# Kernel optimization log

Hardware: AMD Instinct MI355X
Metric: run time of the kernel (lower is better)

Reference implementation:

```python
import jax, jax.numpy as jnp
import numpy as np

N_NODES = 50000
N_EDGES = 800000
HID = 128
N_PROC = 3  # num_layers - 1 processor iterations (shared weights)


def _mlp(x, w1, b1, w2, b2, w3, b3):
    h = jax.nn.relu(x @ w1 + b1)
    h = jax.nn.relu(h @ w2 + b2)
    return h @ w3 + b3


def setup_inputs() -> dict:
    key = jax.random.key(0)
    ks = jax.random.split(key, 32)

    def p(k, shape):
        fan_in = shape[0]
        return (jax.random.normal(k, shape, dtype=jnp.float32) / np.float32(np.sqrt(fan_in)))

    inp = {
        "X_curr": jax.random.normal(ks[0], (N_NODES, 6), dtype=jnp.float32),
        "y_prev": jax.random.normal(ks[1], (N_NODES,), dtype=jnp.float32),
        "edge": jax.random.randint(ks[2], (2, N_EDGES), 0, N_NODES, dtype=jnp.int32),
        "mode": 0,
        # EdgeModel net: Linear(9,H) ReLU Linear(H,H) ReLU Linear(H,3)
        "ew1": p(ks[3], (9, HID)), "eb1": jnp.zeros((HID,), jnp.float32),
        "ew2": p(ks[4], (HID, HID)), "eb2": jnp.zeros((HID,), jnp.float32),
        "ew3": p(ks[5], (HID, 3)), "eb3": jnp.zeros((3,), jnp.float32),
        # NodeModel net: Linear(5,H) ReLU Linear(H,H) ReLU Linear(H,1)
        "nw1": p(ks[6], (5, HID)), "nb1": jnp.zeros((HID,), jnp.float32),
        "nw2": p(ks[7], (HID, HID)), "nb2": jnp.zeros((HID,), jnp.float32),
        "nw3": p(ks[8], (HID, 1)), "nb3": jnp.zeros((1,), jnp.float32),
        # decoder: Linear(5,H) ReLU Linear(H,H) ReLU Linear(H,H) ReLU Linear(H,1)
        "dw1": p(ks[9], (5, HID)), "db1": jnp.zeros((HID,), jnp.float32),
        "dw2": p(ks[10], (HID, HID)), "db2": jnp.zeros((HID,), jnp.float32),
        "dw3": p(ks[11], (HID, HID)), "db3": jnp.zeros((HID,), jnp.float32),
        "dw4": p(ks[12], (HID, 1)), "db4": jnp.zeros((1,), jnp.float32),
    }
    return inp


def reference(X_curr, y_prev,
              ew1, eb1, ew2, eb2, ew3, eb3,
              nw1, nb1, nw2, nb2, nw3, nb3,
              dw1, db1, dw2, db2, dw3, db3, dw4, db4,
              edge, mode):
    n = X_curr.shape[0]
    src_idx, dst_idx = edge[0], edge[1]
    # x_in = cat(X_curr[:, [0,1,2,4]], y_prev)  -> [N, 5]
    x = jnp.concatenate([X_curr[:, jnp.array([0, 1, 2, 4])], y_prev[:, None]], axis=-1)

    # _compute_edge_attr: grad_r = (f_dest - f_src) * disp_r
    xs, xd = x[src_idx], x[dst_idx]
    disp = xd[:, :3] - xs[:, :3]
    edge_attr = (xd[:, 4] - xs[:, 4])[:, None] * disp  # [E, 3]

    # degree for scatter-mean (nodes with no incoming edges aggregate to 0)
    deg = jax.ops.segment_sum(jnp.ones((edge.shape[1],), x.dtype), dst_idx, num_segments=n)
    inv_deg = jnp.where(deg > 0, 1.0 / jnp.maximum(deg, 1.0), 0.0)

    for _ in range(N_PROC):
        # EdgeModel
        xs, xd = x[src_idx], x[dst_idx]
        disp = xd[:, :3] - xs[:, :3]
        norm_r = jnp.linalg.norm(disp, axis=-1, keepdims=True)
        net_in = jnp.concatenate([disp, norm_r, edge_attr, xs[:, 4:5], xd[:, 4:5]], axis=-1)  # [E, 9]
        edge_attr = edge_attr + _mlp(net_in, ew1, eb1, ew2, eb2, ew3, eb3)
        # NodeModel: message = edge_attr, aggr='mean' at target (edge[1])
        aggr = jax.ops.segment_sum(edge_attr, dst_idx, num_segments=n) * inv_deg[:, None]  # [N, 3]
        node_in = jnp.concatenate([x[:, 3:5], aggr], axis=-1)  # [N, 5]
        delta = _mlp(node_in, nw1, nb1, nw2, nb2, nw3, nb3)[:, 0]
        x = x.at[:, 4].add(delta)

    # decoder
    h = jax.nn.relu(x @ dw1 + db1)
    h = jax.nn.relu(h @ dw2 + db2)
    h = jax.nn.relu(h @ dw3 + db3)
    x_out = h @ dw4 + db4  # [N, 1]
    return y_prev + x_out[:, 0]
```

## Files before the change

kernel.cpp:

```cpp
#include <hip/hip_runtime.h>

typedef float f32x4 __attribute__((ext_vector_type(4)));
typedef __bf16 bf16x8 __attribute__((ext_vector_type(8)));
typedef __bf16 bf16x4 __attribute__((ext_vector_type(4)));

#define WB_W1E 0
#define WB_W2E 4096
#define WB_W3E 20480
#define WB_W1N 22528
#define WB_W2N 26624
#define WB_W3N 43008
#define WB_W1D 45056
#define WB_W2D 49152
#define WB_W3D 65536
#define WB_W4D 81920
#define WB_TOTAL 83968

#define BKT_SHIFT 6
#define BKT_SZ 64

__global__ void k_prep(const float* __restrict__ ew1, const float* __restrict__ eb1,
                       const float* __restrict__ ew2, const float* __restrict__ ew3,
                       const float* __restrict__ nw1, const float* __restrict__ nb1,
                       const float* __restrict__ nw2, const float* __restrict__ nw3,
                       const float* __restrict__ dw1, const float* __restrict__ db1,
                       const float* __restrict__ dw2, const float* __restrict__ dw3,
                       const float* __restrict__ dw4, __bf16* __restrict__ wb) {
  int gid = blockIdx.x * 256 + threadIdx.x;
  if (gid >= WB_TOTAL) return;
  const float* srcs[10] = {ew1, ew2, ew3, nw1, nw2, nw3, dw1, dw2, dw3, dw4};
  const float* brow[10] = {eb1, 0, 0, nb1, 0, 0, db1, 0, 0, 0};
  const int Ks[10] = {9, 128, 128, 5, 128, 128, 5, 128, 128, 128};
  const int Ns[10] = {128, 128, 3, 128, 128, 1, 128, 128, 128, 1};
  const int CTs[10] = {8, 8, 1, 8, 8, 1, 8, 8, 8, 1};
  const int cum[11] = {0, 4096, 20480, 22528, 26624, 43008, 45056, 49152, 65536, 81920, 83968};
  int seg = 0;
  while (gid >= cum[seg + 1]) seg++;
  int li = gid - cum[seg];
  int j = li & 7;
  int lane = (li >> 3) & 63;
  int fi = li >> 9;
  int CT = CTs[seg];
  int ct = fi % CT;
  int kt = fi / CT;
  int k = kt * 32 + ((lane >> 4) << 3) + j;
  int n = ct * 16 + (lane & 15);
  int kl;
  if (seg == 0) {
    if (k < 4) kl = k;
    else if (k >= 8 && k < 13) kl = k - 4;
    else kl = (k == 13) ? -2 : -1;
  } else if (seg == 3 || seg == 6) {
    if (k < 5) kl = k;
    else kl = (k == 5) ? -2 : -1;
  } else {
    kl = (k < Ks[seg]) ? k : -1;
  }
  float v = 0.f;
  if (n < Ns[seg]) {
    if (kl >= 0) v = srcs[seg][kl * Ns[seg] + n];
    else if (kl == -2 && brow[seg]) v = brow[seg][n];
  }
  wb[gid] = (__bf16)v;
}

__global__ void k_zero(const float* __restrict__ y_prev, float* __restrict__ x4,
                       int* __restrict__ bcnt, int n, int nbkt) {
  int i = blockIdx.x * 256 + threadIdx.x;
  if (i < n) x4[i] = y_prev[i];
  if (i <= nbkt) bcnt[i] = 0;
}

__global__ __launch_bounds__(256) void k_cntb(const int* __restrict__ dstp,
                                              int* __restrict__ bcnt, int nbkt, int E) {
  __shared__ int hist[1024];
  int tid = threadIdx.x;
  for (int t = tid; t < nbkt; t += 256) hist[t] = 0;
  __syncthreads();
  int e0 = blockIdx.x * 8192;
#pragma unroll
  for (int j = 0; j < 32; j++) {
    int e = e0 + j * 256 + tid;
    if (e < E) atomicAdd(&hist[dstp[e] >> BKT_SHIFT], 1);
  }
  __syncthreads();
  for (int t = tid; t < nbkt; t += 256) {
    int c = hist[t];
    if (c) atomicAdd(&bcnt[t], c);
  }
}

__global__ void k_scanb(const int* __restrict__ bcnt, int* __restrict__ bstart,
                        int* __restrict__ cur, int* __restrict__ rp, int nbkt, int n, int E) {
  __shared__ int sd[1024];
  int t = threadIdx.x;
  int c = (t < nbkt) ? bcnt[t] : 0;
  sd[t] = c;
  __syncthreads();
#pragma unroll
  for (int off = 1; off < 1024; off <<= 1) {
    int v = sd[t];
    int u = (t >= off) ? sd[t - off] : 0;
    __syncthreads();
    sd[t] = v + u;
    __syncthreads();
  }
  if (t < nbkt) {
    int ex = sd[t] - c;
    bstart[t] = ex;
    cur[t] = ex;
  }
  if (t == 0) {
    bstart[nbkt] = E;
    rp[n] = E;
  }
}

__global__ __launch_bounds__(256) void k_bin(const int* __restrict__ dstp, int* __restrict__ cur,
                                             int* __restrict__ eix, int nbkt, int E) {
  __shared__ int hist[1024];
  __shared__ int base[1024];
  int tid = threadIdx.x;
  for (int t = tid; t < nbkt; t += 256) hist[t] = 0;
  __syncthreads();
  int e0 = blockIdx.x * 8192;
  int b[32], lr[32];
#pragma unroll
  for (int j = 0; j < 32; j++) {
    int e = e0 + j * 256 + tid;
    if (e < E) {
      b[j] = dstp[e] >> BKT_SHIFT;
      lr[j] = atomicAdd(&hist[b[j]], 1);
    } else {
      b[j] = -1;
      lr[j] = 0;
    }
  }
  __syncthreads();
  for (int t = tid; t < nbkt; t += 256) {
    int c = hist[t];
    base[t] = c ? atomicAdd(&cur[t], c) : 0;
  }
  __syncthreads();
#pragma unroll
  for (int j = 0; j < 32; j++)
    if (b[j] >= 0) eix[base[b[j]] + lr[j]] = e0 + j * 256 + tid;
}

__global__ __launch_bounds__(256) void k_build(const int* __restrict__ srcO,
                                               const int* __restrict__ dstO,
                                               const float* __restrict__ Xc,
                                               const float* __restrict__ yp,
                                               const int* __restrict__ bstart, const int* eix,
                                               int* __restrict__ srcS, int* dstS,
                                               float* __restrict__ peS, float* __restrict__ eaS,
                                               int* __restrict__ rp, float* __restrict__ invdeg,
                                               int n) {
  __shared__ int cnt[BKT_SZ];
  __shared__ int starts[BKT_SZ];
  int tid = threadIdx.x;
  int d0 = blockIdx.x << BKT_SHIFT;
  if (tid < BKT_SZ) cnt[tid] = 0;
  int gstart = bstart[blockIdx.x], gend = bstart[blockIdx.x + 1];
  __syncthreads();
  int ei[16], dd[16], rr[16];
#pragma unroll
  for (int k = 0; k < 16; k++) {
    int p = gstart + k * 256 + tid;
    ei[k] = (p < gend) ? eix[p] : -1;
  }
#pragma unroll
  for (int k = 0; k < 16; k++) {
    if (ei[k] >= 0) {
      dd[k] = dstO[ei[k]];
      rr[k] = atomicAdd(&cnt[dd[k] - d0], 1);
    }
  }
  __syncthreads();
  if (tid < 64) {
    int c = cnt[tid];
    int s = c;
#pragma unroll
    for (int off = 1; off < 64; off <<= 1) {
      int u = __shfl_up(s, off);
      if (tid >= off) s += u;
    }
    int ex = s - c;
    starts[tid] = ex;
    int d = d0 + tid;
    if (d < n) {
      rp[d] = gstart + ex;
      invdeg[d] = c > 0 ? 1.0f / (float)c : 0.f;
    }
  }
  __syncthreads();
#pragma unroll
  for (int k = 0; k < 16; k++) {
    int e = ei[k];
    if (e < 0) continue;
    int s = srcO[e], d = dd[k];
    float dx = Xc[d * 6 + 0] - Xc[s * 6 + 0];
    float dy = Xc[d * 6 + 1] - Xc[s * 6 + 1];
    float dz = Xc[d * 6 + 2] - Xc[s * 6 + 2];
    float nr = sqrtf(dx * dx + dy * dy + dz * dz);
    float w = yp[d] - yp[s];
    int q = gstart + starts[d - d0] + rr[k];
    srcS[q] = s;
    dstS[q] = d;
    f32x4 pv = {dx, dy, dz, nr};
    *(f32x4*)(peS + 4 * q) = pv;
    f32x4 av = {w * dx, w * dy, w * dz, 0.f};
    *(f32x4*)(eaS + 4 * q) = av;
  }
}

__device__ __forceinline__ int aoff(int row, int b) { return (row * 256 + b) ^ ((row & 15) << 4); }

__device__ __forceinline__ void wg_sync() {
  asm volatile("s_waitcnt lgkmcnt(0)" ::: "memory");
  __builtin_amdgcn_s_barrier();
}

__device__ __forceinline__ bf16x4 relu_pack(f32x4 a) {
  bf16x4 p;
#pragma unroll
  for (int r = 0; r < 4; r++) {
    float v = a[r];
    p[r] = (__bf16)(v > 0.f ? v : 0.f);
  }
  return p;
}

__global__ __attribute__((amdgpu_flat_work_group_size(256, 256), amdgpu_waves_per_eu(3, 4))) void
k_edge(const float* __restrict__ x4, const float* __restrict__ pe, float* __restrict__ ea,
       const int* __restrict__ src, const int* __restrict__ dstp,
       const __bf16* __restrict__ W1f, const __bf16* __restrict__ W2f,
       const __bf16* __restrict__ W3f, const float* __restrict__ b2,
       const float* __restrict__ b3, int ntiles, int E) {
  __shared__ char Ab[16384];
  __shared__ char Bb[16384];
  const int tid = threadIdx.x;
  const int l = tid & 63, w = tid >> 6;
  const int col = l & 15, krow = l >> 4;
  const int rl = w * 16 + (l >> 2), chunk = l & 3;

  bf16x8 w1r[2], w2r[4][2], w3r[4];
#pragma unroll
  for (int t = 0; t < 2; t++) w1r[t] = *(const bf16x8*)(W1f + ((2 * w + t) << 9) + l * 8);
#pragma unroll
  for (int kt = 0; kt < 4; kt++)
#pragma unroll
    for (int t = 0; t < 2; t++)
      w2r[kt][t] = *(const bf16x8*)(W2f + ((kt * 8 + 2 * w + t) << 9) + l * 8);
#pragma unroll
  for (int kt = 0; kt < 4; kt++) w3r[kt] = *(const bf16x8*)(W3f + (kt << 9) + l * 8);
  f32x4 b2c[2];
#pragma unroll
  for (int t = 0; t < 2; t++) b2c[t] = *(const f32x4*)(b2 + (2 * w + t) * 16 + krow * 4);
  f32x4 b3i = {0.f, 0.f, 0.f, 0.f};
  if (krow == 0) {
    b3i[0] = b3[0];
    b3i[1] = b3[1];
    b3i[2] = b3[2];
  }

  int tile = blockIdx.x;
  if (tile >= ntiles) return;

  int e0 = tile * 64 + rl;
  int ec = e0 < E ? e0 : E - 1;
  int cs = src[ec], cd = dstp[ec];
  f32x4 cld = {0.f, 0.f, 0.f, 0.f};
  if (chunk < 2) cld = *(const f32x4*)(((chunk == 1) ? ea : pe) + 4 * ec);
  float cxs = 0.f, cxd = 0.f;
  if (chunk == 1) {
    cxs = x4[cs];
    cxd = x4[cd];
  }

  for (;;) {
    bf16x8 v;
#pragma unroll
    for (int q = 0; q < 8; q++) v[q] = (__bf16)0.f;
    if (chunk == 0) {
      v[0] = (__bf16)cld[0];
      v[1] = (__bf16)cld[1];
      v[2] = (__bf16)cld[2];
      v[3] = (__bf16)cld[3];
    } else if (chunk == 1) {
      v[0] = (__bf16)cld[0];
      v[1] = (__bf16)cld[1];
      v[2] = (__bf16)cld[2];
      v[3] = (__bf16)cxs;
      v[4] = (__bf16)cxd;
      v[5] = (__bf16)1.0f;
    }
    *(bf16x8*)(Ab + aoff(rl, chunk * 16)) = v;

    int nt = tile + (int)gridDim.x;
    bool hn = nt < ntiles;
    int tc = hn ? nt : tile;
    int en = tc * 64 + rl;
    if (en >= E) en = E - 1;
    int ns = src[en], nd = dstp[en];

    wg_sync();

    f32x4 h[4][2];
#pragma unroll
    for (int c = 0; c < 4; c++)
#pragma unroll
      for (int t = 0; t < 2; t++) {
        f32x4 z = {0.f, 0.f, 0.f, 0.f};
        h[c][t] = z;
      }
    bf16x8 bb[4];
#pragma unroll
    for (int c = 0; c < 4; c++) bb[c] = *(const bf16x8*)(Ab + aoff(c * 16 + col, krow * 16));
#pragma unroll
    for (int c = 0; c < 4; c++)
#pragma unroll
      for (int t = 0; t < 2; t++)
        h[c][t] = __builtin_amdgcn_mfma_f32_16x16x32_bf16(w1r[t], bb[c], h[c][t], 0, 0, 0);
#pragma unroll
    for (int c = 0; c < 4; c++)
#pragma unroll
      for (int t = 0; t < 2; t++)
        *(bf16x4*)(Bb + aoff(c * 16 + col, (2 * w + t) * 32 + krow * 8)) = relu_pack(h[c][t]);

    wg_sync();

    f32x4 nld = {0.f, 0.f, 0.f, 0.f};
    if (chunk < 2) nld = *(const f32x4*)(((chunk == 1) ? ea : pe) + 4 * en);
    float nxs = 0.f, nxd = 0.f;
    if (chunk == 1) {
      nxs = x4[ns];
      nxd = x4[nd];
    }

#pragma unroll
    for (int c = 0; c < 4; c++)
#pragma unroll
      for (int t = 0; t < 2; t++) h[c][t] = b2c[t];
#pragma unroll
    for (int kt = 0; kt < 4; kt++) {
#pragma unroll
      for (int c = 0; c < 4; c++)
        bb[c] = *(const bf16x8*)(Bb + aoff(c * 16 + col, kt * 64 + krow * 16));
#pragma unroll
      for (int c = 0; c < 4; c++)
#pragma unroll
        for (int t = 0; t < 2; t++)
          h[c][t] = __builtin_amdgcn_mfma_f32_16x16x32_bf16(w2r[kt][t], bb[c], h[c][t], 0, 0, 0);
    }
#pragma unroll
    for (int c = 0; c < 4; c++)
#pragma unroll
      for (int t = 0; t < 2; t++)
        *(bf16x4*)(Ab + aoff(c * 16 + col, (2 * w + t) * 32 + krow * 8)) = relu_pack(h[c][t]);

    wg_sync();

    f32x4 o = b3i;
#pragma unroll
    for (int kt = 0; kt < 4; kt++) {
      bf16x8 bq = *(const bf16x8*)(Ab + aoff(w * 16 + col, kt * 64 + krow * 16));
      o = __builtin_amdgcn_mfma_f32_16x16x32_bf16(w3r[kt], bq, o, 0, 0, 0);
    }

    if (krow == 0) {
      int e3 = tile * 64 + w * 16 + col;
      if (e3 < E) {
        f32x4 oe = *(const f32x4*)(ea + 4 * e3);
        f32x4 nv;
        nv[0] = oe[0] + o[0];
        nv[1] = oe[1] + o[1];
        nv[2] = oe[2] + o[2];
        nv[3] = 0.f;
        *(f32x4*)(ea + 4 * e3) = nv;
      }
    }

    if (!hn) break;
    tile = nt;
    cld = nld;
    cxs = nxs;
    cxd = nxd;
  }
}

__global__ __attribute__((amdgpu_flat_work_group_size(256, 256), amdgpu_waves_per_eu(3, 4))) void
k_node(float* __restrict__ x4, const float* __restrict__ Xc, const float* __restrict__ eaS,
       const int* __restrict__ rp, const float* __restrict__ invdeg,
       const __bf16* __restrict__ W1f, const __bf16* __restrict__ W2f,
       const __bf16* __restrict__ W3f, const float* __restrict__ b2,
       const float* __restrict__ b3, int n) {
  __shared__ char Ab[16384];
  __shared__ char Bb[16384];
  const int tid = threadIdx.x;
  const int l = tid & 63, w = tid >> 6;
  const int col = l & 15, krow = l >> 4;
  const int rl = w * 16 + (l >> 2), chunk = l & 3;

  bf16x8 w1r[2], w2r[4][2], w3r[4];
#pragma unroll
  for (int t = 0; t < 2; t++) w1r[t] = *(const bf16x8*)(W1f + ((2 * w + t) << 9) + l * 8);
#pragma unroll
  for (int kt = 0; kt < 4; kt++)
#pragma unroll
    for (int t = 0; t < 2; t++)
      w2r[kt][t] = *(const bf16x8*)(W2f + ((kt * 8 + 2 * w + t) << 9) + l * 8);
#pragma unroll
  for (int kt = 0; kt < 4; kt++) w3r[kt] = *(const bf16x8*)(W3f + (kt << 9) + l * 8);
  f32x4 b2c[2];
#pragma unroll
  for (int t = 0; t < 2; t++) b2c[t] = *(const f32x4*)(b2 + (2 * w + t) * 16 + krow * 4);
  float b3s = b3[0];

  int tile = blockIdx.x;
  int i0 = tile * 64 + rl;
  bool vi = i0 < n;
  int i = vi ? i0 : (n - 1);

  int ss = rp[i], se = rp[i + 1];
  float a0 = 0.f, a1 = 0.f, a2 = 0.f;
  for (int p = ss + chunk; p < se; p += 4) {
    f32x4 ev = *(const f32x4*)(eaS + 4 * p);
    a0 += ev[0];
    a1 += ev[1];
    a2 += ev[2];
  }
  a0 += __shfl_xor(a0, 1);
  a1 += __shfl_xor(a1, 1);
  a2 += __shfl_xor(a2, 1);
  a0 += __shfl_xor(a0, 2);
  a1 += __shfl_xor(a1, 2);
  a2 += __shfl_xor(a2, 2);

  bf16x8 v;
#pragma unroll
  for (int q = 0; q < 8; q++) v[q] = (__bf16)0.f;
  if (chunk == 0) {
    float x3 = Xc[i * 6 + 4];
    float xv = x4[i];
    float iv = invdeg[i];
    v[0] = (__bf16)x3;
    v[1] = (__bf16)xv;
    v[2] = (__bf16)(a0 * iv);
    v[3] = (__bf16)(a1 * iv);
    v[4] = (__bf16)(a2 * iv);
    v[5] = (__bf16)1.0f;
  }
  *(bf16x8*)(Ab + aoff(rl, chunk * 16)) = v;

  wg_sync();

  f32x4 h[4][2];
#pragma unroll
  for (int c = 0; c < 4; c++)
#pragma unroll
    for (int t = 0; t < 2; t++) {
      f32x4 z = {0.f, 0.f, 0.f, 0.f};
      h[c][t] = z;
    }
  bf16x8 bb[4];
#pragma unroll
  for (int c = 0; c < 4; c++) bb[c] = *(const bf16x8*)(Ab + aoff(c * 16 + col, krow * 16));
#pragma unroll
  for (int c = 0; c < 4; c++)
#pragma unroll
    for (int t = 0; t < 2; t++)
      h[c][t] = __builtin_amdgcn_mfma_f32_16x16x32_bf16(w1r[t], bb[c], h[c][t], 0, 0, 0);
#pragma unroll
  for (int c = 0; c < 4; c++)
#pragma unroll
    for (int t = 0; t < 2; t++)
      *(bf16x4*)(Bb + aoff(c * 16 + col, (2 * w + t) * 32 + krow * 8)) = relu_pack(h[c][t]);

  wg_sync();

#pragma unroll
  for (int c = 0; c < 4; c++)
#pragma unroll
    for (int t = 0; t < 2; t++) h[c][t] = b2c[t];
#pragma unroll
  for (int kt = 0; kt < 4; kt++) {
#pragma unroll
    for (int c = 0; c < 4; c++)
      bb[c] = *(const bf16x8*)(Bb + aoff(c * 16 + col, kt * 64 + krow * 16));
#pragma unroll
    for (int c = 0; c < 4; c++)
#pragma unroll
      for (int t = 0; t < 2; t++)
        h[c][t] = __builtin_amdgcn_mfma_f32_16x16x32_bf16(w2r[kt][t], bb[c], h[c][t], 0, 0, 0);
  }
#pragma unroll
  for (int c = 0; c < 4; c++)
#pragma unroll
    for (int t = 0; t < 2; t++)
      *(bf16x4*)(Ab + aoff(c * 16 + col, (2 * w + t) * 32 + krow * 8)) = relu_pack(h[c][t]);

  wg_sync();

  f32x4 o = {0.f, 0.f, 0.f, 0.f};
  if (krow == 0) o[0] = b3s;
#pragma unroll
  for (int kt = 0; kt < 4; kt++) {
    bf16x8 bq = *(const bf16x8*)(Ab + aoff(w * 16 + col, kt * 64 + krow * 16));
    o = __builtin_amdgcn_mfma_f32_16x16x32_bf16(w3r[kt], bq, o, 0, 0, 0);
  }

  if (krow == 0) {
    int i3 = tile * 64 + w * 16 + col;
    if (i3 < n) x4[i3] = x4[i3] + o[0];
  }
}

__global__ __attribute__((amdgpu_flat_work_group_size(256, 256), amdgpu_waves_per_eu(2, 4))) void
k_dec(const float* __restrict__ x4, const float* __restrict__ Xc, const float* __restrict__ y_prev,
      const __bf16* __restrict__ W1f, const __bf16* __restrict__ W2f,
      const __bf16* __restrict__ W3f, const __bf16* __restrict__ W4f,
      const float* __restrict__ b2, const float* __restrict__ b3, const float* __restrict__ b4,
      float* __restrict__ out, int n) {
  __shared__ char Ab[16384];
  __shared__ char Bb[16384];
  const int tid = threadIdx.x;
  const int l = tid & 63, w = tid >> 6;
  const int col = l & 15, krow = l >> 4;
  const int rl = w * 16 + (l >> 2), chunk = l & 3;

  bf16x8 w1r[2], w2r[4][2], w3r[4][2], w4r[4];
#pragma unroll
  for (int t = 0; t < 2; t++) w1r[t] = *(const bf16x8*)(W1f + ((2 * w + t) << 9) + l * 8);
#pragma unroll
  for (int kt = 0; kt < 4; kt++)
#pragma unroll
    for (int t = 0; t < 2; t++) {
      w2r[kt][t] = *(const bf16x8*)(W2f + ((kt * 8 + 2 * w + t) << 9) + l * 8);
      w3r[kt][t] = *(const bf16x8*)(W3f + ((kt * 8 + 2 * w + t) << 9) + l * 8);
    }
#pragma unroll
  for (int kt = 0; kt < 4; kt++) w4r[kt] = *(const bf16x8*)(W4f + (kt << 9) + l * 8);
  f32x4 b2c[2], b3c[2];
#pragma unroll
  for (int t = 0; t < 2; t++) {
    b2c[t] = *(const f32x4*)(b2 + (2 * w + t) * 16 + krow * 4);
    b3c[t] = *(const f32x4*)(b3 + (2 * w + t) * 16 + krow * 4);
  }
  float b4s = b4[0];

  int tile = blockIdx.x;
  int i0 = tile * 64 + rl;
  bool vi = i0 < n;
  int i = vi ? i0 : (n - 1);

  bf16x8 v;
#pragma unroll
  for (int q = 0; q < 8; q++) v[q] = (__bf16)0.f;
  if (chunk == 0) {
    v[0] = (__bf16)Xc[i * 6 + 0];
    v[1] = (__bf16)Xc[i * 6 + 1];
    v[2] = (__bf16)Xc[i * 6 + 2];
    v[3] = (__bf16)Xc[i * 6 + 4];
    v[4] = (__bf16)x4[i];
    v[5] = (__bf16)1.0f;
  }
  *(bf16x8*)(Ab + aoff(rl, chunk * 16)) = v;

  wg_sync();

  f32x4 h[4][2];
  bf16x8 bb[4];
#pragma unroll
  for (int c = 0; c < 4; c++)
#pragma unroll
    for (int t = 0; t < 2; t++) {
      f32x4 z = {0.f, 0.f, 0.f, 0.f};
      h[c][t] = z;
    }
#pragma unroll
  for (int c = 0; c < 4; c++) bb[c] = *(const bf16x8*)(Ab + aoff(c * 16 + col, krow * 16));
#pragma unroll
  for (int c = 0; c < 4; c++)
#pragma unroll
    for (int t = 0; t < 2; t++)
      h[c][t] = __builtin_amdgcn_mfma_f32_16x16x32_bf16(w1r[t], bb[c], h[c][t], 0, 0, 0);
#pragma unroll
  for (int c = 0; c < 4; c++)
#pragma unroll
    for (int t = 0; t < 2; t++)
      *(bf16x4*)(Bb + aoff(c * 16 + col, (2 * w + t) * 32 + krow * 8)) = relu_pack(h[c][t]);

  wg_sync();

#pragma unroll
  for (int c = 0; c < 4; c++)
#pragma unroll
    for (int t = 0; t < 2; t++) h[c][t] = b2c[t];
#pragma unroll
  for (int kt = 0; kt < 4; kt++) {
#pragma unroll
    for (int c = 0; c < 4; c++)
      bb[c] = *(const bf16x8*)(Bb + aoff(c * 16 + col, kt * 64 + krow * 16));
#pragma unroll
    for (int c = 0; c < 4; c++)
#pragma unroll
      for (int t = 0; t < 2; t++)
        h[c][t] = __builtin_amdgcn_mfma_f32_16x16x32_bf16(w2r[kt][t], bb[c], h[c][t], 0, 0, 0);
  }
#pragma unroll
  for (int c = 0; c < 4; c++)
#pragma unroll
    for (int t = 0; t < 2; t++)
      *(bf16x4*)(Ab + aoff(c * 16 + col, (2 * w + t) * 32 + krow * 8)) = relu_pack(h[c][t]);

  wg_sync();

#pragma unroll
  for (int c = 0; c < 4; c++)
#pragma unroll
    for (int t = 0; t < 2; t++) h[c][t] = b3c[t];
#pragma unroll
  for (int kt = 0; kt < 4; kt++) {
#pragma unroll
    for (int c = 0; c < 4; c++)
      bb[c] = *(const bf16x8*)(Ab + aoff(c * 16 + col, kt * 64 + krow * 16));
#pragma unroll
    for (int c = 0; c < 4; c++)
#pragma unroll
      for (int t = 0; t < 2; t++)
        h[c][t] = __builtin_amdgcn_mfma_f32_16x16x32_bf16(w3r[kt][t], bb[c], h[c][t], 0, 0, 0);
  }
#pragma unroll
  for (int c = 0; c < 4; c++)
#pragma unroll
    for (int t = 0; t < 2; t++)
      *(bf16x4*)(Bb + aoff(c * 16 + col, (2 * w + t) * 32 + krow * 8)) = relu_pack(h[c][t]);

  wg_sync();

  f32x4 o = {0.f, 0.f, 0.f, 0.f};
  if (krow == 0) o[0] = b4s;
#pragma unroll
  for (int kt = 0; kt < 4; kt++) {
    bf16x8 bq = *(const bf16x8*)(Bb + aoff(w * 16 + col, kt * 64 + krow * 16));
    o = __builtin_amdgcn_mfma_f32_16x16x32_bf16(w4r[kt], bq, o, 0, 0, 0);
  }

  if (krow == 0) {
    int i3 = tile * 64 + w * 16 + col;
    if (i3 < n) out[i3] = y_prev[i3] + o[0];
  }
}

extern "C" void kernel_launch(void* const* d_in, const int* in_sizes, int n_in, void* d_out,
                              int out_size, void* d_ws, size_t ws_size, hipStream_t stream) {
  const float* Xc = (const float*)d_in[0];
  const float* y_prev = (const float*)d_in[1];
  const int* edge = (const int*)d_in[2];
  const float* ew1 = (const float*)d_in[4];
  const float* eb1 = (const float*)d_in[5];
  const float* ew2 = (const float*)d_in[6];
  const float* eb2 = (const float*)d_in[7];
  const float* ew3 = (const float*)d_in[8];
  const float* eb3 = (const float*)d_in[9];
  const float* nw1 = (const float*)d_in[10];
  const float* nb1 = (const float*)d_in[11];
  const float* nw2 = (const float*)d_in[12];
  const float* nb2 = (const float*)d_in[13];
  const float* nw3 = (const float*)d_in[14];
  const float* nb3 = (const float*)d_in[15];
  const float* dw1 = (const float*)d_in[16];
  const float* db1 = (const float*)d_in[17];
  const float* dw2 = (const float*)d_in[18];
  const float* db2 = (const float*)d_in[19];
  const float* dw3 = (const float*)d_in[20];
  const float* db3 = (const float*)d_in[21];
  const float* dw4 = (const float*)d_in[22];
  const float* db4 = (const float*)d_in[23];

  int n = in_sizes[0] / 6;
  int E = in_sizes[2] / 2;
  const int* srcp = edge;
  const int* dstp = edge + E;

  __bf16* wb = (__bf16*)d_ws;
  float* fbase = (float*)((char*)d_ws + (size_t)WB_TOTAL * 2);
  size_t na = ((size_t)n + 3) & ~(size_t)3;
  float* x4 = fbase;
  float* invdeg = fbase + na;
  int* rp = (int*)(fbase + 2 * na);
  int* bcnt = rp + na + 8;
  int* bstart = bcnt + 1056;
  int* cur = bstart + 1056;
  int* srcS = cur + 1024;
  int* dstS = srcS + E;
  float* peS = (float*)(dstS + E);
  float* eaS = peS + 4 * (size_t)E;

  size_t need = (size_t)WB_TOTAL * 2 + (3 * na + 8 + 3136 + 10 * (size_t)E) * 4;
  if (ws_size < need) return;

  dim3 B(256);
  int nblk = (n + 255) / 256;
  int nbkt = (n + BKT_SZ - 1) / BKT_SZ;
  int eblk = (E + 8191) / 8192;
  k_prep<<<dim3((WB_TOTAL + 255) / 256), B, 0, stream>>>(ew1, eb1, ew2, ew3, nw1, nb1, nw2, nw3,
                                                         dw1, db1, dw2, dw3, dw4, wb);
  k_zero<<<dim3(nblk), B, 0, stream>>>(y_prev, x4, bcnt, n, nbkt);
  k_cntb<<<dim3(eblk), B, 0, stream>>>(dstp, bcnt, nbkt, E);
  k_scanb<<<dim3(1), dim3(1024), 0, stream>>>(bcnt, bstart, cur, rp, nbkt, n, E);
  k_bin<<<dim3(eblk), B, 0, stream>>>(dstp, cur, dstS, nbkt, E);
  k_build<<<dim3(nbkt), B, 0, stream>>>(srcp, dstp, Xc, y_prev, bstart, dstS, srcS, dstS, peS,
                                        eaS, rp, invdeg, n);

  int etiles = (E + 63) / 64;
  int vtiles = (n + 63) / 64;
  int egrid = etiles < 512 ? etiles : 512;
  for (int it = 0; it < 3; it++) {
    k_edge<<<dim3(egrid), B, 0, stream>>>(x4, peS, eaS, srcS, dstS, wb + WB_W1E, wb + WB_W2E,
                                          wb + WB_W3E, eb2, eb3, etiles, E);
    k_node<<<dim3(vtiles), B, 0, stream>>>(x4, Xc, eaS, rp, invdeg, wb + WB_W1N, wb + WB_W2N,
                                           wb + WB_W3N, nb2, nb3, n);
  }
  k_dec<<<dim3(vtiles), B, 0, stream>>>(x4, Xc, y_prev, wb + WB_W1D, wb + WB_W2D, wb + WB_W3D,
                                        wb + WB_W4D, db2, db3, db4, (float*)d_out, n);
}
```

Measured before the change: 275.7 us.

## Halve edge tile to 32 rows to raise occupancy and grid size

The edge MLP kernel now processes 32 edges per tile instead of 64. LDS buffers shrink to 8 KB each, register arrays are halved, and waves_per_eu is raised to 4-8 so more blocks fit per CU. Only half the lanes stage inputs, and only two waves run the final layer. The grid cap goes from 512 to 2048 persistent blocks, and an extra barrier at the end of each loop iteration guards LDS reuse. The aim is better latency hiding for the gather loads, paid for with more barriers per edge and lower MFMA work per sync.

After: 267.3 us. -3.0%, faster.

```diff
diff --git a/kernel.cpp b/kernel.cpp
--- a/kernel.cpp
+++ b/kernel.cpp
@@ -231,18 +231,19 @@
   return p;
 }
 
-__global__ __attribute__((amdgpu_flat_work_group_size(256, 256), amdgpu_waves_per_eu(3, 4))) void
+__global__ __attribute__((amdgpu_flat_work_group_size(256, 256), amdgpu_waves_per_eu(4, 8))) void
 k_edge(const float* __restrict__ x4, const float* __restrict__ pe, float* __restrict__ ea,
        const int* __restrict__ src, const int* __restrict__ dstp,
        const __bf16* __restrict__ W1f, const __bf16* __restrict__ W2f,
        const __bf16* __restrict__ W3f, const float* __restrict__ b2,
        const float* __restrict__ b3, int ntiles, int E) {
-  __shared__ char Ab[16384];
-  __shared__ char Bb[16384];
+  __shared__ char Ab[8192];
+  __shared__ char Bb[8192];
   const int tid = threadIdx.x;
   const int l = tid & 63, w = tid >> 6;
   const int col = l & 15, krow = l >> 4;
-  const int rl = w * 16 + (l >> 2), chunk = l & 3;
+  const int rl = w * 8 + (l >> 2), chunk = l & 3;
+  const bool stager = l < 32;
 
   bf16x8 w1r[2], w2r[4][2], w3r[4];
 #pragma unroll
@@ -258,7 +259,7 @@
 #pragma unroll
   for (int t = 0; t < 2; t++) b2c[t] = *(const f32x4*)(b2 + (2 * w + t) * 16 + krow * 4);
   f32x4 b3i = {0.f, 0.f, 0.f, 0.f};
-  if (krow == 0) {
+  if (w < 2 && krow == 0) {
     b3i[0] = b3[0];
     b3i[1] = b3[1];
     b3i[2] = b3[2];
@@ -267,63 +268,65 @@
   int tile = blockIdx.x;
   if (tile >= ntiles) return;
 
-  int e0 = tile * 64 + rl;
+  int e0 = tile * 32 + rl;
   int ec = e0 < E ? e0 : E - 1;
-  int cs = src[ec], cd = dstp[ec];
   f32x4 cld = {0.f, 0.f, 0.f, 0.f};
-  if (chunk < 2) cld = *(const f32x4*)(((chunk == 1) ? ea : pe) + 4 * ec);
   float cxs = 0.f, cxd = 0.f;
-  if (chunk == 1) {
-    cxs = x4[cs];
-    cxd = x4[cd];
+  if (stager) {
+    if (chunk < 2) cld = *(const f32x4*)(((chunk == 1) ? ea : pe) + 4 * ec);
+    if (chunk == 1) {
+      cxs = x4[src[ec]];
+      cxd = x4[dstp[ec]];
+    }
   }
 
   for (;;) {
-    bf16x8 v;
-#pragma unroll
-    for (int q = 0; q < 8; q++) v[q] = (__bf16)0.f;
-    if (chunk == 0) {
-      v[0] = (__bf16)cld[0];
-      v[1] = (__bf16)cld[1];
-      v[2] = (__bf16)cld[2];
-      v[3] = (__bf16)cld[3];
-    } else if (chunk == 1) {
-      v[0] = (__bf16)cld[0];
-      v[1] = (__bf16)cld[1];
-      v[2] = (__bf16)cld[2];
-      v[3] = (__bf16)cxs;
-      v[4] = (__bf16)cxd;
-      v[5] = (__bf16)1.0f;
-    }
-    *(bf16x8*)(Ab + aoff(rl, chunk * 16)) = v;
+    if (stager) {
+      bf16x8 v;
+#pragma unroll
+      for (int q = 0; q < 8; q++) v[q] = (__bf16)0.f;
+      if (chunk == 0) {
+        v[0] = (__bf16)cld[0];
+        v[1] = (__bf16)cld[1];
+        v[2] = (__bf16)cld[2];
+        v[3] = (__bf16)cld[3];
+      } else if (chunk == 1) {
+        v[0] = (__bf16)cld[0];
+        v[1] = (__bf16)cld[1];
+        v[2] = (__bf16)cld[2];
+        v[3] = (__bf16)cxs;
+        v[4] = (__bf16)cxd;
+        v[5] = (__bf16)1.0f;
+      }
+      *(bf16x8*)(Ab + aoff(rl, chunk * 16)) = v;
+    }
 
     int nt = tile + (int)gridDim.x;
     bool hn = nt < ntiles;
     int tc = hn ? nt : tile;
-    int en = tc * 64 + rl;
+    int en = tc * 32 + rl;
     if (en >= E) en = E - 1;
-    int ns = src[en], nd = dstp[en];
+    int ns = 0, nd = 0;
+    if (stager && chunk == 1) {
+      ns = src[en];
+      nd = dstp[en];
+    }
 
     wg_sync();
 
-    f32x4 h[4][2];
-#pragma unroll
-    for (int c = 0; c < 4; c++)
+    f32x4 h[2][2];
+    bf16x8 bb[2];
+#pragma unroll
+    for (int c = 0; c < 2; c++) bb[c] = *(const bf16x8*)(Ab + aoff(c * 16 + col, krow * 16));
+#pragma unroll
+    for (int c = 0; c < 2; c++)
 #pragma unroll
       for (int t = 0; t < 2; t++) {
         f32x4 z = {0.f, 0.f, 0.f, 0.f};
-        h[c][t] = z;
+        h[c][t] = __builtin_amdgcn_mfma_f32_16x16x32_bf16(w1r[t], bb[c], z, 0, 0, 0);
       }
-    bf16x8 bb[4];
-#pragma unroll
-    for (int c = 0; c < 4; c++) bb[c] = *(const bf16x8*)(Ab + aoff(c * 16 + col, krow * 16));
-#pragma unroll
-    for (int c = 0; c < 4; c++)
-#pragma unroll
-      for (int t = 0; t < 2; t++)
-        h[c][t] = __builtin_amdgcn_mfma_f32_16x16x32_bf16(w1r[t], bb[c], h[c][t], 0, 0, 0);
-#pragma unroll
-    for (int c = 0; c < 4; c++)
+#pragma unroll
+    for (int c = 0; c < 2; c++)
 #pragma unroll
       for (int t = 0; t < 2; t++)
         *(bf16x4*)(Bb + aoff(c * 16 + col, (2 * w + t) * 32 + krow * 8)) = relu_pack(h[c][t]);
@@ -331,53 +334,56 @@
     wg_sync();
 
     f32x4 nld = {0.f, 0.f, 0.f, 0.f};
-    if (chunk < 2) nld = *(const f32x4*)(((chunk == 1) ? ea : pe) + 4 * en);
     float nxs = 0.f, nxd = 0.f;
-    if (chunk == 1) {
-      nxs = x4[ns];
-      nxd = x4[nd];
-    }
-
-#pragma unroll
-    for (int c = 0; c < 4; c++)
+    if (stager) {
+      if (chunk < 2) nld = *(const f32x4*)(((chunk == 1) ? ea : pe) + 4 * en);
+      if (chunk == 1) {
+        nxs = x4[ns];
+        nxd = x4[nd];
+      }
+    }
+
+#pragma unroll
+    for (int c = 0; c < 2; c++)
 #pragma unroll
       for (int t = 0; t < 2; t++) h[c][t] = b2c[t];
 #pragma unroll
     for (int kt = 0; kt < 4; kt++) {
 #pragma unroll
-      for (int c = 0; c < 4; c++)
+      for (int c = 0; c < 2; c++)
         bb[c] = *(const bf16x8*)(Bb + aoff(c * 16 + col, kt * 64 + krow * 16));
 #pragma unroll
-      for (int c = 0; c < 4; c++)
+      for (int c = 0; c < 2; c++)
 #pragma unroll
         for (int t = 0; t < 2; t++)
           h[c][t] = __builtin_amdgcn_mfma_f32_16x16x32_bf16(w2r[kt][t], bb[c], h[c][t], 0, 0, 0);
     }
 #pragma unroll
-    for (int c = 0; c < 4; c++)
+    for (int c = 0; c < 2; c++)
 #pragma unroll
       for (int t = 0; t < 2; t++)
         *(bf16x4*)(Ab + aoff(c * 16 + col, (2 * w + t) * 32 + krow * 8)) = relu_pack(h[c][t]);
 
     wg_sync();
 
-    f32x4 o = b3i;
-#pragma unroll
-    for (int kt = 0; kt < 4; kt++) {
-      bf16x8 bq = *(const bf16x8*)(Ab + aoff(w * 16 + col, kt * 64 + krow * 16));
-      o = __builtin_amdgcn_mfma_f32_16x16x32_bf16(w3r[kt], bq, o, 0, 0, 0);
-    }
-
-    if (krow == 0) {
-      int e3 = tile * 64 + w * 16 + col;
-      if (e3 < E) {
-        f32x4 oe = *(const f32x4*)(ea + 4 * e3);
-        f32x4 nv;
-        nv[0] = oe[0] + o[0];
-        nv[1] = oe[1] + o[1];
-        nv[2] = oe[2] + o[2];
-        nv[3] = 0.f;
-        *(f32x4*)(ea + 4 * e3) = nv;
+    if (w < 2) {
+      f32x4 o = b3i;
+#pragma unroll
+      for (int kt = 0; kt < 4; kt++) {
+        bf16x8 bq = *(const bf16x8*)(Ab + aoff(w * 16 + col, kt * 64 + krow * 16));
+        o = __builtin_amdgcn_mfma_f32_16x16x32_bf16(w3r[kt], bq, o, 0, 0, 0);
+      }
+      if (krow == 0) {
+        int e3 = tile * 32 + w * 16 + col;
+        if (e3 < E) {
+          f32x4 oe = *(const f32x4*)(ea + 4 * e3);
+          f32x4 nv;
+          nv[0] = oe[0] + o[0];
+          nv[1] = oe[1] + o[1];
+          nv[2] = oe[2] + o[2];
+          nv[3] = 0.f;
+          *(f32x4*)(ea + 4 * e3) = nv;
+        }
       }
     }
 
@@ -386,6 +392,7 @@
     cld = nld;
     cxs = nxs;
     cxd = nxd;
+    wg_sync();
   }
 }
 
@@ -714,9 +721,9 @@
   k_build<<<dim3(nbkt), B, 0, stream>>>(srcp, dstp, Xc, y_prev, bstart, dstS, srcS, dstS, peS,
                                         eaS, rp, invdeg, n);
 
-  int etiles = (E + 63) / 64;
+  int etiles = (E + 31) / 32;
   int vtiles = (n + 63) / 64;
-  int egrid = etiles < 512 ? etiles : 512;
+  int egrid = etiles < 2048 ? etiles : 2048;
   for (int it = 0; it < 3; it++) {
     k_edge<<<dim3(egrid), B, 0, stream>>>(x4, peS, eaS, srcS, dstS, wb + WB_W1E, wb + WB_W2E,
                                           wb + WB_W3E, eb2, eb3, etiles, E);
```
